# Optimization experiments

Measured on AMD Instinct MI355X. Metric: run time of the kernel, lower is better.

The kernel has to match this reference:

```python
import jax, jax.numpy as jnp
import numpy as np
from jax import lax

WINDOW_SIZE = 11
SIGMA = 1.5
IMG_RANGE = 2.0
MS_WEIGHTS = np.array([0.0448, 0.2856, 0.3001, 0.2363, 0.1333], dtype=np.float32)


def _gauss_window(k=WINDOW_SIZE, sigma=SIGMA):
    x = np.arange(k, dtype=np.float64) - k // 2
    g = np.exp(-(x ** 2) / (2.0 * sigma ** 2))
    g = g / g.sum()
    return jnp.asarray(np.outer(g, g), dtype=jnp.float32)  # [k, k]


def _dwconv(x, win):
    # depthwise valid conv, groups = channels (torch conv2d weight [C,1,k,k])
    c = x.shape[1]
    k = win.shape[0]
    rhs = jnp.broadcast_to(win[None, None], (c, 1, k, k))
    return lax.conv_general_dilated(
        x, rhs, window_strides=(1, 1), padding='VALID',
        dimension_numbers=('NCHW', 'OIHW', 'NCHW'), feature_group_count=c)


def _ssim(img1, img2, win, img_range):
    mu1 = _dwconv(img1, win)
    mu2 = _dwconv(img2, win)
    mu1_sq, mu2_sq, mu1_mu2 = mu1 * mu1, mu2 * mu2, mu1 * mu2
    sigma1_sq = _dwconv(img1 * img1, win) - mu1_sq
    sigma2_sq = _dwconv(img2 * img2, win) - mu2_sq
    sigma12 = _dwconv(img1 * img2, win) - mu1_mu2
    C1 = (0.01 * img_range) ** 2
    C2 = (0.03 * img_range) ** 2
    v1 = 2.0 * sigma12 + C2
    v2 = sigma1_sq + sigma2_sq + C2
    cs = jnp.mean(v1 / v2)
    ssim_map = (2.0 * mu1_mu2 + C1) * v1 / ((mu1_sq + mu2_sq + C1) * v2)
    return jnp.mean(ssim_map), cs


def _avg_pool2(x):
    b, c, h, w = x.shape
    return x.reshape(b, c, h // 2, 2, w // 2, 2).mean(axis=(3, 5))


def _msssim_loss(img1, img2):
    win = _gauss_window()
    weights = jnp.asarray(MS_WEIGHTS)
    sims = []
    mcs = None
    for _ in range(len(MS_WEIGHTS)):  # fixed 5 pyramid levels
        sim, mcs = _ssim(img1, img2, win, IMG_RANGE)
        sims.append(sim)
        img1 = _avg_pool2(img1)
        img2 = _avg_pool2(img2)
    ssims = jnp.stack(sims)
    # faithful to source: cs from LAST level powered by weights[-1]
    output = mcs ** weights[-1] * jnp.prod(ssims ** weights)
    return 1.0 - output


def setup_inputs() -> dict:
    key = jax.random.key(0)
    k1, k2 = jax.random.split(key)
    img1 = jax.random.normal(k1, (16, 3, 512, 512), dtype=jnp.float32)
    # correlated pair so per-level SSIM/CS means stay positive (fractional powers)
    img2 = img1 + 0.05 * jax.random.normal(k2, (16, 3, 512, 512), dtype=jnp.float32)
    return {'img1': img1, 'img2': img2}


def reference(img1, img2):
    return _msssim_loss(img1, img2)
```

## Files before the change

kernel.cpp:

```cpp
#include <hip/hip_runtime.h>
#include <math.h>

typedef float vf2 __attribute__((ext_vector_type(2)));

#define NB0 12288
#define NB1 3072
#define NB2 768
#define NB3 192
#define NB4 48
#define NPART 16368

__global__ void msssim_init_kernel(float* __restrict__ g) {
    if (threadIdx.x == 0) {
        double w[11]; double s = 0.0;
        for (int i = 0; i < 11; ++i) { double x = (double)(i - 5); w[i] = exp(-(x * x) / 4.5); s += w[i]; }
        for (int i = 0; i < 11; ++i) g[i] = (float)(w[i] / s);
    }
}

struct Smem {
    float4 sAB2[21][43];
    float4 vrt[16][45];
    float red[8];
};

template<int F>
__device__ __forceinline__ float poolrec(const float* __restrict__ p, int Y, int X) {
    if constexpr (F == 2) {
        float2 r0 = *(const float2*)(p + (size_t)Y * 256 + X);
        float2 r1 = *(const float2*)(p + (size_t)(Y + 1) * 256 + X);
        return 0.25f * ((r0.x + r0.y) + (r1.x + r1.y));
    } else {
        constexpr int H = F / 2;
        return 0.25f * ((poolrec<H>(p, Y, X) + poolrec<H>(p, Y, X + H))
                      + (poolrec<H>(p, Y + H, X) + poolrec<H>(p, Y + H, X + H)));
    }
}

template<int J>
__device__ __forceinline__ void vtap(vf2 m, const float (&g)[11], vf2 (&amu)[4], vf2 (&aq)[4]) {
    vf2 t = m * m;
    vf2 q = { t.x + t.y, m.x * m.y };
#pragma unroll
    for (int i = 0; i < 4; ++i) {
        if (J - i >= 0 && J - i <= 10) {
            vf2 gs = { g[J - i], g[J - i] };
            amu[i] = __builtin_elementwise_fma(gs, m, amu[i]);
            aq[i]  = __builtin_elementwise_fma(gs, q, aq[i]);
        }
    }
}

template<int T>
__device__ __forceinline__ void htap(const float4 V, const float (&g)[11], vf2 (&amu)[4], vf2 (&aq)[4]) {
    vf2 mt = { V.x, V.y }, qt = { V.z, V.w };
#pragma unroll
    for (int i = 0; i < 4; ++i) {
        if (T - i >= 0 && T - i <= 10) {
            vf2 gs = { g[T - i], g[T - i] };
            amu[i] = __builtin_elementwise_fma(gs, mt, amu[i]);
            aq[i]  = __builtin_elementwise_fma(gs, qt, aq[i]);
        }
    }
}

template<int L>
__device__ __forceinline__ void ssim_body(Smem& sm, int tbx, int tby, int z,
    const float* __restrict__ i1, const float* __restrict__ i2,
    const float* __restrict__ gg, float2* __restrict__ partials, int pidx,
    float* __restrict__ o1, float* __restrict__ o2)
{
    constexpr int Hl = 512 >> L;
    constexpr int Hv = Hl - 10;
    const int tid = threadIdx.x;
    const int bx = tbx * 32, by = tby * 32;

    float g[11];
#pragma unroll
    for (int j = 0; j < 11; ++j) g[j] = gg[j];

    if constexpr (L <= 1) {
        const float* p1 = i1 + (size_t)z * Hl * Hl;
        const float* p2 = i2 + (size_t)z * Hl * Hl;
        for (int i = tid; i < 441; i += 256) {
            int rp = i / 21, cp = i - rp * 21, c = 2 * cp;
            int y = by + 2 * rp, x = bx + c;
            float2 a0 = {0.f,0.f}, a1 = a0, b0 = a0, b1 = a0;
            if (y < Hl && x < Hl) {
                const float* r1p = p1 + (size_t)y * Hl + x;
                a0 = *(const float2*)r1p;
                a1 = *(const float2*)(r1p + Hl);
                const float* r2p = p2 + (size_t)y * Hl + x;
                b0 = *(const float2*)r2p;
                b1 = *(const float2*)(r2p + Hl);
            }
            sm.sAB2[rp][c]     = make_float4(a0.x, b0.x, a1.x, b1.x);
            sm.sAB2[rp][c + 1] = make_float4(a0.y, b0.y, a1.y, b1.y);
        }
    } else {
        constexpr int F = 1 << (L - 1);
        const float* p1 = i1 + (size_t)z * 65536;
        const float* p2 = i2 + (size_t)z * 65536;
        for (int i = tid; i < 441; i += 256) {
            int rp = i / 21, cp = i - rp * 21, c = 2 * cp;
            int ly = by + 2 * rp, lx = bx + c;
            float a00=0.f,a01=0.f,a10=0.f,a11=0.f,b00=0.f,b01=0.f,b10=0.f,b11=0.f;
            if (ly < Hl && lx < Hl) {
                int Y = ly * F, X = lx * F;
                a00 = poolrec<F>(p1, Y, X);         b00 = poolrec<F>(p2, Y, X);
                a01 = poolrec<F>(p1, Y, X + F);     b01 = poolrec<F>(p2, Y, X + F);
                a10 = poolrec<F>(p1, Y + F, X);     b10 = poolrec<F>(p2, Y + F, X);
                a11 = poolrec<F>(p1, Y + F, X + F); b11 = poolrec<F>(p2, Y + F, X + F);
            }
            sm.sAB2[rp][c]     = make_float4(a00, b00, a10, b10);
            sm.sAB2[rp][c + 1] = make_float4(a01, b01, a11, b11);
        }
    }
    __syncthreads();

    if constexpr (L == 0) {
        int py = tid >> 4, px = tid & 15;
        float4 q0 = sm.sAB2[py][2 * px];
        float4 q1 = sm.sAB2[py][2 * px + 1];
        size_t po = (size_t)z * 65536 + (size_t)(tby * 16 + py) * 256 + (tbx * 16 + px);
        o1[po] = 0.25f * ((q0.x + q1.x) + (q0.z + q1.z));
        o2[po] = 0.25f * ((q0.y + q1.y) + (q0.w + q1.w));
    }

    float ssim_l = 0.f, cs_l = 0.f;

#pragma unroll
    for (int p = 0; p < 2; ++p) {
        if (p) __syncthreads();

        if (tid < 168) {
            int c = tid % 42, ch = tid / 42;
            int rp0 = 8 * p + 2 * ch;
            vf2 amu[4], aq[4];
#pragma unroll
            for (int i = 0; i < 4; ++i) { amu[i] = (vf2){0.f,0.f}; aq[i] = (vf2){0.f,0.f}; }
#define VPAIR(K) { float4 Q = sm.sAB2[rp0 + (K)][c];                  \
                   vtap<2*(K)>((vf2){Q.x, Q.y}, g, amu, aq);          \
                   vtap<2*(K)+1>((vf2){Q.z, Q.w}, g, amu, aq); }
            VPAIR(0) VPAIR(1) VPAIR(2) VPAIR(3) VPAIR(4) VPAIR(5) VPAIR(6)
#undef VPAIR
            int r0 = 4 * ch;
#pragma unroll
            for (int i = 0; i < 4; ++i)
                sm.vrt[r0 + i][c] = make_float4(amu[i].x, amu[i].y, aq[i].x, aq[i].y);
        }
        __syncthreads();

        if (tid < 128) {
            int row = tid >> 3, oct = tid & 7, c0 = 4 * oct;
            int oy = by + 16 * p + row;
            vf2 amu[4], aq[4];
#pragma unroll
            for (int i = 0; i < 4; ++i) { amu[i] = (vf2){0.f,0.f}; aq[i] = (vf2){0.f,0.f}; }
#define HT(T) htap<(T)>(sm.vrt[row][c0 + (T)], g, amu, aq);
            HT(0) HT(1) HT(2) HT(3) HT(4) HT(5) HT(6)
            HT(7) HT(8) HT(9) HT(10) HT(11) HT(12) HT(13)
#undef HT
            if (oy < Hv) {
#pragma unroll
                for (int i = 0; i < 4; ++i) {
                    int ox = bx + c0 + i;
                    if (ox < Hv) {
                        vf2 mu = amu[i], qq = aq[i];
                        float ab = mu.x * mu.y;
                        vf2 t = mu * mu;
                        float aabb = t.x + t.y;
                        float n1 = fmaf(2.f, ab, 0.0004f);
                        float d1 = aabb + 0.0004f;
                        float v1 = fmaf(2.f, qq.y - ab, 0.0036f);
                        float v2 = (qq.x - aabb) + 0.0036f;
                        float rden = __builtin_amdgcn_rcpf(d1 * v2);
                        cs_l   = fmaf(v1 * d1, rden, cs_l);
                        ssim_l = fmaf(n1 * v1, rden, ssim_l);
                    }
                }
            }
        }
    }

#pragma unroll
    for (int off = 32; off > 0; off >>= 1) {
        ssim_l += __shfl_down(ssim_l, off);
        cs_l   += __shfl_down(cs_l, off);
    }
    int wave = tid >> 6, lane = tid & 63;
    if (lane == 0) { sm.red[wave] = ssim_l; sm.red[4 + wave] = cs_l; }
    __syncthreads();
    if (tid == 0) {
        float ss = sm.red[0] + sm.red[1] + sm.red[2] + sm.red[3];
        float cc = sm.red[4] + sm.red[5] + sm.red[6] + sm.red[7];
        partials[pidx] = make_float2(ss, cc);
    }
}

__global__ __launch_bounds__(256, 6) void ssim_l0_kernel(
    const float* __restrict__ img1, const float* __restrict__ img2,
    const float* __restrict__ gg, float2* __restrict__ partials,
    float* __restrict__ o1, float* __restrict__ o2)
{
    __shared__ Smem sm;
    int pidx = ((int)blockIdx.z * 16 + (int)blockIdx.y) * 16 + (int)blockIdx.x;
    ssim_body<0>(sm, blockIdx.x, blockIdx.y, blockIdx.z, img1, img2, gg, partials, pidx, o1, o2);
}

__global__ __launch_bounds__(256, 6) void ssim_rest_kernel(
    const float* __restrict__ L1a, const float* __restrict__ L1b,
    const float* __restrict__ gg, float2* __restrict__ partials)
{
    __shared__ Smem sm;
    int b = blockIdx.x;
    if (b < 3072) {
        int lb = b;        int z = lb >> 6; int r = lb & 63; int tby = r >> 3; int tbx = r & 7;
        ssim_body<1>(sm, tbx, tby, z, L1a, L1b, gg, partials, 12288 + lb, nullptr, nullptr);
    } else if (b < 3840) {
        int lb = b - 3072; int z = lb >> 4; int r = lb & 15; int tby = r >> 2; int tbx = r & 3;
        ssim_body<2>(sm, tbx, tby, z, L1a, L1b, gg, partials, 15360 + lb, nullptr, nullptr);
    } else if (b < 4032) {
        int lb = b - 3840; int z = lb >> 2; int r = lb & 3;  int tby = r >> 1; int tbx = r & 1;
        ssim_body<3>(sm, tbx, tby, z, L1a, L1b, gg, partials, 16128 + lb, nullptr, nullptr);
    } else {
        int lb = b - 4032;
        ssim_body<4>(sm, 0, 0, lb, L1a, L1b, gg, partials, 16320 + lb, nullptr, nullptr);
    }
}

__global__ __launch_bounds__(1024) void msssim_reduce_kernel(
    const float2* __restrict__ partials, float* __restrict__ out)
{
    __shared__ double sred[16][2];
    __shared__ double lev[10];
    const int NB[5]  = {NB0, NB1, NB2, NB3, NB4};
    const int OFF[5] = {0, NB0, NB0 + NB1, NB0 + NB1 + NB2, NB0 + NB1 + NB2 + NB3};
    const int tid = threadIdx.x;
    const int wv = tid >> 6, ln = tid & 63;

    for (int l = 0; l < 5; ++l) {
        double s = 0.0, c = 0.0;
        for (int i = tid; i < NB[l]; i += 1024) {
            float2 p = partials[OFF[l] + i];
            s += (double)p.x; c += (double)p.y;
        }
#pragma unroll
        for (int off = 32; off > 0; off >>= 1) {
            s += __shfl_down(s, off);
            c += __shfl_down(c, off);
        }
        if (ln == 0) { sred[wv][0] = s; sred[wv][1] = c; }
        __syncthreads();
        if (tid == 0) {
            double ss = 0.0, cc = 0.0;
            for (int w = 0; w < 16; ++w) { ss += sred[w][0]; cc += sred[w][1]; }
            lev[l] = ss; lev[5 + l] = cc;
        }
        __syncthreads();
    }

    if (tid == 0) {
        const double counts[5] = {
            48.0 * 502.0 * 502.0,
            48.0 * 246.0 * 246.0,
            48.0 * 118.0 * 118.0,
            48.0 * 54.0 * 54.0,
            48.0 * 22.0 * 22.0
        };
        const double w[5] = { (double)0.0448f, (double)0.2856f, (double)0.3001f,
                              (double)0.2363f, (double)0.1333f };
        double prod = 1.0;
        for (int i = 0; i < 5; ++i) prod *= pow(lev[i] / counts[i], w[i]);
        double mcs = lev[9] / counts[4];
        double output = pow(mcs, w[4]) * prod;
        out[0] = (float)(1.0 - output);
    }
}

extern "C" void kernel_launch(void* const* d_in, const int* in_sizes, int n_in,
                              void* d_out, int out_size, void* d_ws, size_t ws_size,
                              hipStream_t stream) {
    const float* img1 = (const float*)d_in[0];
    const float* img2 = (const float*)d_in[1];
    float* out = (float*)d_out;

    char* ws = (char*)d_ws;
    float* g = (float*)ws;
    float2* partials = (float2*)(ws + 256);
    float* Aw1 = (float*)(ws + 256 + 131072);
    float* Bw1 = Aw1 + (size_t)48 * 65536;

    msssim_init_kernel<<<dim3(1), dim3(64), 0, stream>>>(g);

    ssim_l0_kernel<<<dim3(16, 16, 48), dim3(256), 0, stream>>>(
        img1, img2, g, partials, Aw1, Bw1);

    ssim_rest_kernel<<<dim3(4080), dim3(256), 0, stream>>>(Aw1, Bw1, g, partials);

    msssim_reduce_kernel<<<dim3(1), dim3(1024), 0, stream>>>(partials, out);
}
```

Measured before the change: 230.5 us.

## Build full image pyramid in level-0 kernel and pass Gaussian weights as kernel argument

Measured after the change: 197.5 us. -14.4%, faster.

```diff
diff --git a/kernel.cpp b/kernel.cpp
--- a/kernel.cpp
+++ b/kernel.cpp
@@ -1,7 +1,9 @@
 #include <hip/hip_runtime.h>
-#include <math.h>
+#include <cmath>
 
 typedef float vf2 __attribute__((ext_vector_type(2)));
+
+struct G11 { float v[11]; };
 
 #define NB0 12288
 #define NB1 3072
@@ -10,33 +12,12 @@
 #define NB4 48
 #define NPART 16368
 
-__global__ void msssim_init_kernel(float* __restrict__ g) {
-    if (threadIdx.x == 0) {
-        double w[11]; double s = 0.0;
-        for (int i = 0; i < 11; ++i) { double x = (double)(i - 5); w[i] = exp(-(x * x) / 4.5); s += w[i]; }
-        for (int i = 0; i < 11; ++i) g[i] = (float)(w[i] / s);
-    }
-}
-
 struct Smem {
     float4 sAB2[21][43];
     float4 vrt[16][45];
     float red[8];
 };
 
-template<int F>
-__device__ __forceinline__ float poolrec(const float* __restrict__ p, int Y, int X) {
-    if constexpr (F == 2) {
-        float2 r0 = *(const float2*)(p + (size_t)Y * 256 + X);
-        float2 r1 = *(const float2*)(p + (size_t)(Y + 1) * 256 + X);
-        return 0.25f * ((r0.x + r0.y) + (r1.x + r1.y));
-    } else {
-        constexpr int H = F / 2;
-        return 0.25f * ((poolrec<H>(p, Y, X) + poolrec<H>(p, Y, X + H))
-                      + (poolrec<H>(p, Y + H, X) + poolrec<H>(p, Y + H, X + H)));
-    }
-}
-
 template<int J>
 __device__ __forceinline__ void vtap(vf2 m, const float (&g)[11], vf2 (&amu)[4], vf2 (&aq)[4]) {
     vf2 t = m * m;
@@ -64,11 +45,14 @@
     }
 }
 
+struct PyrOut {
+    float *a1, *b1, *a2, *b2, *a3, *b3, *a4, *b4;
+};
+
 template<int L>
 __device__ __forceinline__ void ssim_body(Smem& sm, int tbx, int tby, int z,
     const float* __restrict__ i1, const float* __restrict__ i2,
-    const float* __restrict__ gg, float2* __restrict__ partials, int pidx,
-    float* __restrict__ o1, float* __restrict__ o2)
+    const G11 gw, float2* __restrict__ partials, int pidx, const PyrOut* po)
 {
     constexpr int Hl = 512 >> L;
     constexpr int Hv = Hl - 10;
@@ -77,9 +61,9 @@
 
     float g[11];
 #pragma unroll
-    for (int j = 0; j < 11; ++j) g[j] = gg[j];
-
-    if constexpr (L <= 1) {
+    for (int j = 0; j < 11; ++j) g[j] = gw.v[j];
+
+    {
         const float* p1 = i1 + (size_t)z * Hl * Hl;
         const float* p2 = i2 + (size_t)z * Hl * Hl;
         for (int i = tid; i < 441; i += 256) {
@@ -97,34 +81,55 @@
             sm.sAB2[rp][c]     = make_float4(a0.x, b0.x, a1.x, b1.x);
             sm.sAB2[rp][c + 1] = make_float4(a0.y, b0.y, a1.y, b1.y);
         }
-    } else {
-        constexpr int F = 1 << (L - 1);
-        const float* p1 = i1 + (size_t)z * 65536;
-        const float* p2 = i2 + (size_t)z * 65536;
-        for (int i = tid; i < 441; i += 256) {
-            int rp = i / 21, cp = i - rp * 21, c = 2 * cp;
-            int ly = by + 2 * rp, lx = bx + c;
-            float a00=0.f,a01=0.f,a10=0.f,a11=0.f,b00=0.f,b01=0.f,b10=0.f,b11=0.f;
-            if (ly < Hl && lx < Hl) {
-                int Y = ly * F, X = lx * F;
-                a00 = poolrec<F>(p1, Y, X);         b00 = poolrec<F>(p2, Y, X);
-                a01 = poolrec<F>(p1, Y, X + F);     b01 = poolrec<F>(p2, Y, X + F);
-                a10 = poolrec<F>(p1, Y + F, X);     b10 = poolrec<F>(p2, Y + F, X);
-                a11 = poolrec<F>(p1, Y + F, X + F); b11 = poolrec<F>(p2, Y + F, X + F);
+    }
+    __syncthreads();
+
+    if constexpr (L == 0) {
+        float2* pp = (float2*)&sm.vrt[0][0];
+        {
+            int py = tid >> 4, px = tid & 15;
+            float4 q0 = sm.sAB2[py][2 * px];
+            float4 q1 = sm.sAB2[py][2 * px + 1];
+            float l1a = 0.25f * ((q0.x + q1.x) + (q0.z + q1.z));
+            float l1b = 0.25f * ((q0.y + q1.y) + (q0.w + q1.w));
+            size_t o = (size_t)z * 65536 + (size_t)(tby * 16 + py) * 256 + (tbx * 16 + px);
+            po->a1[o] = l1a; po->b1[o] = l1b;
+            pp[tid] = make_float2(l1a, l1b);
+        }
+        __syncthreads();
+        if (tid < 64) {
+            int y = tid >> 3, x = tid & 7;
+            float2 p00 = pp[(2*y)*16 + 2*x],     p01 = pp[(2*y)*16 + 2*x + 1];
+            float2 p10 = pp[(2*y+1)*16 + 2*x],   p11 = pp[(2*y+1)*16 + 2*x + 1];
+            float l2a = 0.25f * ((p00.x + p01.x) + (p10.x + p11.x));
+            float l2b = 0.25f * ((p00.y + p01.y) + (p10.y + p11.y));
+            size_t o2 = (size_t)z * 16384 + (size_t)(tby * 8 + y) * 128 + (tbx * 8 + x);
+            po->a2[o2] = l2a; po->b2[o2] = l2b;
+
+            int b3 = (16 * (tid >> 2) + 2 * (tid & 3)) & 63;
+            float a00 = __shfl(l2a, b3),     a01 = __shfl(l2a, b3 + 1);
+            float a10 = __shfl(l2a, b3 + 8), a11 = __shfl(l2a, b3 + 9);
+            float c00 = __shfl(l2b, b3),     c01 = __shfl(l2b, b3 + 1);
+            float c10 = __shfl(l2b, b3 + 8), c11 = __shfl(l2b, b3 + 9);
+            float l3a = 0.25f * ((a00 + a01) + (a10 + a11));
+            float l3b = 0.25f * ((c00 + c01) + (c10 + c11));
+            if (tid < 16) {
+                size_t o3 = (size_t)z * 4096 + (size_t)(tby * 4 + (tid >> 2)) * 64 + (tbx * 4 + (tid & 3));
+                po->a3[o3] = l3a; po->b3[o3] = l3b;
             }
-            sm.sAB2[rp][c]     = make_float4(a00, b00, a10, b10);
-            sm.sAB2[rp][c + 1] = make_float4(a01, b01, a11, b11);
-        }
-    }
-    __syncthreads();
-
-    if constexpr (L == 0) {
-        int py = tid >> 4, px = tid & 15;
-        float4 q0 = sm.sAB2[py][2 * px];
-        float4 q1 = sm.sAB2[py][2 * px + 1];
-        size_t po = (size_t)z * 65536 + (size_t)(tby * 16 + py) * 256 + (tbx * 16 + px);
-        o1[po] = 0.25f * ((q0.x + q1.x) + (q0.z + q1.z));
-        o2[po] = 0.25f * ((q0.y + q1.y) + (q0.w + q1.w));
+            int b4 = (8 * (tid >> 1) + 2 * (tid & 1)) & 63;
+            float d00 = __shfl(l3a, b4),     d01 = __shfl(l3a, b4 + 1);
+            float d10 = __shfl(l3a, b4 + 4), d11 = __shfl(l3a, b4 + 5);
+            float e00 = __shfl(l3b, b4),     e01 = __shfl(l3b, b4 + 1);
+            float e10 = __shfl(l3b, b4 + 4), e11 = __shfl(l3b, b4 + 5);
+            float l4a = 0.25f * ((d00 + d01) + (d10 + d11));
+            float l4b = 0.25f * ((e00 + e01) + (e10 + e11));
+            if (tid < 4) {
+                size_t o4 = (size_t)z * 1024 + (size_t)(tby * 2 + (tid >> 1)) * 32 + (tbx * 2 + (tid & 1));
+                po->a4[o4] = l4a; po->b4[o4] = l4b;
+            }
+        }
+        __syncthreads();
     }
 
     float ssim_l = 0.f, cs_l = 0.f;
@@ -200,32 +205,30 @@
 
 __global__ __launch_bounds__(256, 6) void ssim_l0_kernel(
     const float* __restrict__ img1, const float* __restrict__ img2,
-    const float* __restrict__ gg, float2* __restrict__ partials,
-    float* __restrict__ o1, float* __restrict__ o2)
+    const G11 gw, float2* __restrict__ partials, const PyrOut po)
 {
     __shared__ Smem sm;
     int pidx = ((int)blockIdx.z * 16 + (int)blockIdx.y) * 16 + (int)blockIdx.x;
-    ssim_body<0>(sm, blockIdx.x, blockIdx.y, blockIdx.z, img1, img2, gg, partials, pidx, o1, o2);
+    ssim_body<0>(sm, blockIdx.x, blockIdx.y, blockIdx.z, img1, img2, gw, partials, pidx, &po);
 }
 
 __global__ __launch_bounds__(256, 6) void ssim_rest_kernel(
-    const float* __restrict__ L1a, const float* __restrict__ L1b,
-    const float* __restrict__ gg, float2* __restrict__ partials)
+    const G11 gw, float2* __restrict__ partials, const PyrOut po)
 {
     __shared__ Smem sm;
     int b = blockIdx.x;
     if (b < 3072) {
         int lb = b;        int z = lb >> 6; int r = lb & 63; int tby = r >> 3; int tbx = r & 7;
-        ssim_body<1>(sm, tbx, tby, z, L1a, L1b, gg, partials, 12288 + lb, nullptr, nullptr);
+        ssim_body<1>(sm, tbx, tby, z, po.a1, po.b1, gw, partials, 12288 + lb, nullptr);
     } else if (b < 3840) {
         int lb = b - 3072; int z = lb >> 4; int r = lb & 15; int tby = r >> 2; int tbx = r & 3;
-        ssim_body<2>(sm, tbx, tby, z, L1a, L1b, gg, partials, 15360 + lb, nullptr, nullptr);
+        ssim_body<2>(sm, tbx, tby, z, po.a2, po.b2, gw, partials, 15360 + lb, nullptr);
     } else if (b < 4032) {
         int lb = b - 3840; int z = lb >> 2; int r = lb & 3;  int tby = r >> 1; int tbx = r & 1;
-        ssim_body<3>(sm, tbx, tby, z, L1a, L1b, gg, partials, 16128 + lb, nullptr, nullptr);
+        ssim_body<3>(sm, tbx, tby, z, po.a3, po.b3, gw, partials, 16128 + lb, nullptr);
     } else {
         int lb = b - 4032;
-        ssim_body<4>(sm, 0, 0, lb, L1a, L1b, gg, partials, 16320 + lb, nullptr, nullptr);
+        ssim_body<4>(sm, 0, 0, lb, po.a4, po.b4, gw, partials, 16320 + lb, nullptr);
     }
 }
 
@@ -285,18 +288,31 @@
     const float* img2 = (const float*)d_in[1];
     float* out = (float*)d_out;
 
+    G11 gw;
+    {
+        double w[11]; double s = 0.0;
+        for (int i = 0; i < 11; ++i) { double x = (double)(i - 5); w[i] = std::exp(-(x * x) / 4.5); s += w[i]; }
+        for (int i = 0; i < 11; ++i) gw.v[i] = (float)(w[i] / s);
+    }
+
     char* ws = (char*)d_ws;
-    float* g = (float*)ws;
-    float2* partials = (float2*)(ws + 256);
-    float* Aw1 = (float*)(ws + 256 + 131072);
-    float* Bw1 = Aw1 + (size_t)48 * 65536;
-
-    msssim_init_kernel<<<dim3(1), dim3(64), 0, stream>>>(g);
+    float2* partials = (float2*)ws;
+    float* base = (float*)(ws + 131072);
+    PyrOut po;
+    size_t o = 0;
+    po.a1 = base + o; o += (size_t)48 * 65536;
+    po.b1 = base + o; o += (size_t)48 * 65536;
+    po.a2 = base + o; o += (size_t)48 * 16384;
+    po.b2 = base + o; o += (size_t)48 * 16384;
+    po.a3 = base + o; o += (size_t)48 * 4096;
+    po.b3 = base + o; o += (size_t)48 * 4096;
+    po.a4 = base + o; o += (size_t)48 * 1024;
+    po.b4 = base + o; o += (size_t)48 * 1024;
 
     ssim_l0_kernel<<<dim3(16, 16, 48), dim3(256), 0, stream>>>(
-        img1, img2, g, partials, Aw1, Bw1);
-
-    ssim_rest_kernel<<<dim3(4080), dim3(256), 0, stream>>>(Aw1, Bw1, g, partials);
+        img1, img2, gw, partials, po);
+
+    ssim_rest_kernel<<<dim3(4080), dim3(256), 0, stream>>>(gw, partials, po);
 
     msssim_reduce_kernel<<<dim3(1), dim3(1024), 0, stream>>>(partials, out);
 }
```
